# Kernel tuning notes

Hardware: AMD Instinct MI355X
Metric: run time of the kernel (lower is better)

## Reference

```python
import jax, jax.numpy as jnp
import numpy as np

D_MODEL = 1024
N_HEADS = 16
HEAD_DIM = D_MODEL // N_HEADS
D_FF = 4 * D_MODEL
LN_EPS = 1e-5


def setup_inputs() -> dict:
    key = jax.random.key(0)
    ks = jax.random.split(key, 12)
    B, T = 16, 512
    s = lambda fan_in: 1.0 / np.sqrt(fan_in)
    inp = {
        'x': jax.random.normal(ks[0], (B, T, D_MODEL), jnp.float32),
        # torch Linear layout: [out_features, in_features]
        'w_qkv': jax.random.normal(ks[1], (3 * D_MODEL, D_MODEL), jnp.float32) * s(D_MODEL),
        'w_proj': jax.random.normal(ks[2], (D_MODEL, D_MODEL), jnp.float32) * s(D_MODEL),
        'w_ff1': jax.random.normal(ks[3], (D_FF, D_MODEL), jnp.float32) * s(D_MODEL),
        'b_ff1': jax.random.normal(ks[4], (D_FF,), jnp.float32) * 0.02,
        'w_ff2': jax.random.normal(ks[5], (D_MODEL, D_FF), jnp.float32) * s(D_FF),
        'b_ff2': jax.random.normal(ks[6], (D_MODEL,), jnp.float32) * 0.02,
        'ln1_g': jnp.ones((D_MODEL,), jnp.float32),
        'ln1_b': jnp.zeros((D_MODEL,), jnp.float32),
        'ln2_g': jnp.ones((D_MODEL,), jnp.float32),
        'ln2_b': jnp.zeros((D_MODEL,), jnp.float32),
    }
    return inp


def _layernorm(x, g, b):
    mu = jnp.mean(x, axis=-1, keepdims=True)
    var = jnp.var(x, axis=-1, keepdims=True)
    return (x - mu) * jax.lax.rsqrt(var + LN_EPS) * g + b


def _block(x, w_qkv, w_proj, w_ff1, b_ff1, w_ff2, b_ff2, ln1_g, ln1_b, ln2_g, ln2_b):
    B, T, _ = x.shape
    a = _layernorm(x, ln1_g, ln1_b)
    qkv = a @ w_qkv.T  # [B,T,3D]
    q, k, v = jnp.split(qkv, 3, axis=-1)
    # [B,H,T,hd]
    rs = lambda t: t.reshape(B, T, N_HEADS, HEAD_DIM).transpose(0, 2, 1, 3)
    q, k, v = rs(q), rs(k), rs(v)
    scale = HEAD_DIM ** -0.5
    att = jnp.einsum('bhqd,bhkd->bhqk', q, k) * scale
    causal = jnp.tril(jnp.ones((T, T), bool))
    att = jnp.where(causal, att, jnp.float32(-10000.0))
    att = jax.nn.softmax(att, axis=-1)
    out = jnp.einsum('bhqk,bhkd->bhqd', att, v)
    out = out.transpose(0, 2, 1, 3).reshape(B, T, D_MODEL)
    x = x + out @ w_proj.T
    f = _layernorm(x, ln2_g, ln2_b)
    f = jax.nn.gelu(f @ w_ff1.T + b_ff1, approximate=False) @ w_ff2.T + b_ff2
    return x + f


def reference(x, w_qkv, w_proj, w_ff1, b_ff1, w_ff2, b_ff2, ln1_g, ln1_b, ln2_g, ln2_b):
    return _block(x, w_qkv, w_proj, w_ff1, b_ff1, w_ff2, b_ff2, ln1_g, ln1_b, ln2_g, ln2_b)
```

## Files before the change

### kernel.cpp

```cpp
#include <hip/hip_runtime.h>
#include <stdint.h>

typedef __bf16 bf16x8_t __attribute__((ext_vector_type(8)));
typedef float f32x4_t __attribute__((ext_vector_type(4)));
typedef unsigned short ushort8_t __attribute__((ext_vector_type(8)));

#define DEV __device__ __forceinline__

DEV unsigned short f2bf(float f) {
  union { float f; uint32_t u; } v; v.f = f;
  uint32_t r = v.u + 0x7FFFu + ((v.u >> 16) & 1u);
  return (unsigned short)(r >> 16);
}

DEV void gl_lds16(const void* g, void* l) {
  __builtin_amdgcn_global_load_lds(
      (const __attribute__((address_space(1))) void*)g,
      (__attribute__((address_space(3))) void*)l, 16, 0, 0);
}

DEV float gelu_f(float x) {
  const float y = x * 0.7071067811865475f;
  const float ay = fabsf(y);
  const float t = __builtin_amdgcn_rcpf(1.0f + 0.3275911f * ay);
  float p = fmaf(t, 1.061405429f, -1.453152027f);
  p = fmaf(t, p, 1.421413741f);
  p = fmaf(t, p, -0.284496736f);
  p = fmaf(t, p, 0.254829592f);
  p *= t;
  const float e = __expf(-ay * ay);
  float erfv = 1.0f - p * e;
  erfv = copysignf(erfv, y);
  return 0.5f * x * (1.0f + erfv);
}

__global__ __launch_bounds__(256) void cvt_all(const float* __restrict__ w0, unsigned short* __restrict__ o0,
                                               const float* __restrict__ w1, unsigned short* __restrict__ o1,
                                               const float* __restrict__ w2, unsigned short* __restrict__ o2,
                                               const float* __restrict__ w3, unsigned short* __restrict__ o3) {
  int i = blockIdx.x * 256 + threadIdx.x;
  const float* in; unsigned short* outp;
  if (i < 786432) { in = w0; outp = o0; }
  else if (i < 1048576) { in = w1; outp = o1; i -= 786432; }
  else if (i < 2097152) { in = w2; outp = o2; i -= 1048576; }
  else { in = w3; outp = o3; i -= 2097152; }
  float4 v = ((const float4*)in)[i];
  ushort4 o;
  o.x = f2bf(v.x); o.y = f2bf(v.y); o.z = f2bf(v.z); o.w = f2bf(v.w);
  ((ushort4*)outp)[i] = o;
}

__global__ __launch_bounds__(256) void ln_kernel(const float* __restrict__ x,
                                                 const float* __restrict__ g,
                                                 const float* __restrict__ b,
                                                 unsigned short* __restrict__ outp) {
  const int row = blockIdx.x * 4 + (threadIdx.x >> 6);
  const int lane = threadIdx.x & 63;
  const float4* xr = (const float4*)(x + (size_t)row * 1024);
  float4 v[4];
  float s = 0.f, s2 = 0.f;
#pragma unroll
  for (int j = 0; j < 4; ++j) {
    v[j] = xr[j * 64 + lane];
    s += v[j].x + v[j].y + v[j].z + v[j].w;
    s2 += v[j].x * v[j].x + v[j].y * v[j].y + v[j].z * v[j].z + v[j].w * v[j].w;
  }
#pragma unroll
  for (int off = 1; off < 64; off <<= 1) {
    s += __shfl_xor(s, off, 64);
    s2 += __shfl_xor(s2, off, 64);
  }
  const float mu = s * (1.0f / 1024.0f);
  const float var = s2 * (1.0f / 1024.0f) - mu * mu;
  const float rstd = rsqrtf(var + 1e-5f);
  ushort4* orow = (ushort4*)(outp + (size_t)row * 1024);
  const float4* gp = (const float4*)g;
  const float4* bp = (const float4*)b;
#pragma unroll
  for (int j = 0; j < 4; ++j) {
    float4 gv = gp[j * 64 + lane], bv = bp[j * 64 + lane];
    ushort4 o;
    o.x = f2bf((v[j].x - mu) * rstd * gv.x + bv.x);
    o.y = f2bf((v[j].y - mu) * rstd * gv.y + bv.y);
    o.z = f2bf((v[j].z - mu) * rstd * gv.z + bv.z);
    o.w = f2bf((v[j].w - mu) * rstd * gv.w + bv.w);
    orow[j * 64 + lane] = o;
  }
}

template <int MODE>
__global__ __launch_bounds__(256) void gemm_bt(const unsigned short* __restrict__ A,
                                               const unsigned short* __restrict__ B,
                                               float* __restrict__ Cf,
                                               unsigned short* __restrict__ Cb,
                                               const float* __restrict__ bias,
                                               const float* __restrict__ res,
                                               unsigned short* __restrict__ Vt,
                                               int M, int N, int K) {
  __shared__ unsigned short sA[2][128 * 32];
  __shared__ unsigned short sB[2][128 * 32];
  const int tid = threadIdx.x;
  const int w = tid >> 6, lane = tid & 63;
  const int kg = lane >> 4, l16 = lane & 15;
  const int wm = (w & 1) * 64, wn = (w >> 1) * 64;

  const int cid = blockIdx.y * gridDim.x + blockIdx.x;
  const int colBase = (cid >> 6) * 128;
  const int rowBase = (cid & 63) * 128;

  const int sr = tid >> 2;
  const int gc = ((tid & 3) ^ ((sr >> 1) & 3)) * 8;
  const unsigned short* gA = A + (size_t)(rowBase + sr) * K + gc;
  const unsigned short* gB = B + (size_t)(colBase + sr) * K + gc;

  f32x4_t acc[4][4];
#pragma unroll
  for (int mi = 0; mi < 4; ++mi)
#pragma unroll
    for (int ni = 0; ni < 4; ++ni) acc[mi][ni] = (f32x4_t)0.0f;

  int offA[4], offB[4];
  const int pc = (kg ^ ((l16 >> 1) & 3)) * 8;
#pragma unroll
  for (int i = 0; i < 4; ++i) {
    offA[i] = (wm + i * 16 + l16) * 32 + pc;
    offB[i] = (wn + i * 16 + l16) * 32 + pc;
  }

  gl_lds16(gA, &sA[0][tid * 8]);
  gl_lds16(gA + (size_t)64 * K, &sA[0][2048 + tid * 8]);
  gl_lds16(gB, &sB[0][tid * 8]);
  gl_lds16(gB + (size_t)64 * K, &sB[0][2048 + tid * 8]);
  gA += 32; gB += 32;

  const int nk = K >> 5;
  for (int kt = 0; kt < nk; ++kt) {
    __syncthreads();
    if (kt + 1 < nk) {
      const int nb = (kt + 1) & 1;
      gl_lds16(gA, &sA[nb][tid * 8]);
      gl_lds16(gA + (size_t)64 * K, &sA[nb][2048 + tid * 8]);
      gl_lds16(gB, &sB[nb][tid * 8]);
      gl_lds16(gB + (size_t)64 * K, &sB[nb][2048 + tid * 8]);
      gA += 32; gB += 32;
    }
    const int bo = (kt & 1) * (128 * 32);
    bf16x8_t a[4], b[4];
#pragma unroll
    for (int i = 0; i < 4; ++i) a[i] = *(const bf16x8_t*)(&sA[0][0] + bo + offA[i]);
#pragma unroll
    for (int i = 0; i < 4; ++i) b[i] = *(const bf16x8_t*)(&sB[0][0] + bo + offB[i]);
#pragma unroll
    for (int mi = 0; mi < 4; ++mi)
#pragma unroll
      for (int ni = 0; ni < 4; ++ni)
        acc[mi][ni] = __builtin_amdgcn_mfma_f32_16x16x32_bf16(a[mi], b[ni], acc[mi][ni], 0, 0, 0);
  }

#pragma unroll
  for (int mi = 0; mi < 4; ++mi) {
#pragma unroll
    for (int ni = 0; ni < 4; ++ni) {
      const int col = colBase + wn + ni * 16 + l16;
      if (MODE == 0 && colBase >= 2048) {
        const int c2 = col - 2048;
        const int hh = c2 >> 6, dd = c2 & 63;
        const int rw = rowBase + wm + mi * 16 + kg * 4;
        ushort4 pk;
        pk.x = f2bf(acc[mi][ni][0]);
        pk.y = f2bf(acc[mi][ni][1]);
        pk.z = f2bf(acc[mi][ni][2]);
        pk.w = f2bf(acc[mi][ni][3]);
        *(ushort4*)(Vt + (((size_t)(rw >> 9) * 16 + hh) * 64 + dd) * 512 + (rw & 511)) = pk;
        continue;
      }
      float bv = 0.f;
      if (MODE == 2 || MODE == 3) bv = bias[col];
#pragma unroll
      for (int r = 0; r < 4; ++r) {
        const int row = rowBase + wm + mi * 16 + kg * 4 + r;
        const size_t idx = (size_t)row * N + col;
        float v = acc[mi][ni][r];
        if (MODE == 0) {
          Cb[idx] = f2bf(v);
        } else if (MODE == 1) {
          Cf[idx] = v + res[idx];
        } else if (MODE == 2) {
          Cb[idx] = f2bf(gelu_f(v + bv));
        } else {
          Cf[idx] = v + bv + res[idx];
        }
      }
    }
  }
}

__global__ __launch_bounds__(256) void attn_kernel(const unsigned short* __restrict__ qkv,
                                                   const unsigned short* __restrict__ Vt,
                                                   unsigned short* __restrict__ outp) {
  constexpr int D3 = 3072;
  __shared__ unsigned short sQ[128 * 64];
  __shared__ unsigned short sK[64 * 64];
  __shared__ unsigned short sVt[64 * 64];
  __shared__ unsigned short sP[128 * 72];
  const int tid = threadIdx.x;
  const int w = tid >> 6, lane = tid & 63;
  const int kg = lane >> 4, l16 = lane & 15;
  const int qi = blockIdx.x, h = blockIdx.y, bb = blockIdx.z;
  const int t0 = qi * 128;
  const size_t base = (size_t)bb * 512 * D3 + h * 64;

  const int sr = tid >> 3;
  const int sc = ((tid & 7) ^ (sr & 7)) * 8;

  {
    const unsigned short* g = qkv + base + (size_t)(t0 + sr) * D3 + sc;
    unsigned short* l = sQ + tid * 8;
#pragma unroll
    for (int i = 0; i < 4; ++i) gl_lds16(g + (size_t)32 * i * D3, l + 2048 * i);
  }

  const unsigned short* gVbase = Vt + ((size_t)(bb * 16 + h) * 64 + sr) * 512 + sc;

  const int wm = w * 32;
  f32x4_t o[2][4];
  float m_i[2][4], l_i[2][4];
#pragma unroll
  for (int mi = 0; mi < 2; ++mi)
#pragma unroll
    for (int r = 0; r < 4; ++r) { m_i[mi][r] = -1e30f; l_i[mi][r] = 0.f; }
#pragma unroll
  for (int mi = 0; mi < 2; ++mi)
#pragma unroll
    for (int di = 0; di < 4; ++di) o[mi][di] = (f32x4_t)0.0f;

  const int nkt = (qi + 1) * 2;
  for (int kt = 0; kt < nkt; ++kt) {
    const int k0 = kt * 64;
    __syncthreads();
    {
      const unsigned short* g = qkv + base + 1024 + (size_t)(k0 + sr) * D3 + sc;
      unsigned short* l = sK + tid * 8;
      gl_lds16(g, l);
      gl_lds16(g + (size_t)32 * D3, l + 2048);
    }
    {
      const unsigned short* g = gVbase + k0;
      unsigned short* l = sVt + tid * 8;
      gl_lds16(g, l);
      gl_lds16(g + (size_t)32 * 512, l + 2048);
    }
    __syncthreads();

    const bool active = (k0 <= t0 + wm + 31);
    if (active) {
      f32x4_t s[2][4];
#pragma unroll
      for (int mi = 0; mi < 2; ++mi)
#pragma unroll
        for (int ni = 0; ni < 4; ++ni) s[mi][ni] = (f32x4_t)0.0f;
#pragma unroll
      for (int kd = 0; kd < 2; ++kd) {
        bf16x8_t aq[2], bk[4];
#pragma unroll
        for (int mi = 0; mi < 2; ++mi) {
          const int rr = wm + mi * 16 + l16;
          aq[mi] = *(const bf16x8_t*)(sQ + rr * 64 + (((kd * 4 + kg) ^ (l16 & 7)) * 8));
        }
#pragma unroll
        for (int ni = 0; ni < 4; ++ni) {
          const int rr = ni * 16 + l16;
          bk[ni] = *(const bf16x8_t*)(sK + rr * 64 + (((kd * 4 + kg) ^ (l16 & 7)) * 8));
        }
#pragma unroll
        for (int mi = 0; mi < 2; ++mi)
#pragma unroll
          for (int ni = 0; ni < 4; ++ni)
            s[mi][ni] = __builtin_amdgcn_mfma_f32_16x16x32_bf16(aq[mi], bk[ni], s[mi][ni], 0, 0, 0);
      }
#pragma unroll
      for (int mi = 0; mi < 2; ++mi) {
#pragma unroll
        for (int r = 0; r < 4; ++r) {
          const int q = t0 + wm + mi * 16 + kg * 4 + r;
          float mx = -1e30f;
#pragma unroll
          for (int ni = 0; ni < 4; ++ni) {
            const int kk = k0 + ni * 16 + l16;
            float v = s[mi][ni][r] * 0.125f;
            v = (kk <= q) ? v : -10000.0f;
            s[mi][ni][r] = v;
            mx = fmaxf(mx, v);
          }
#pragma unroll
          for (int off = 1; off < 16; off <<= 1) mx = fmaxf(mx, __shfl_xor(mx, off, 64));
          const float mo = m_i[mi][r];
          const float mn = fmaxf(mo, mx);
          const float alpha = __expf(mo - mn);
          float ps = 0.f;
#pragma unroll
          for (int ni = 0; ni < 4; ++ni) {
            float p = __expf(s[mi][ni][r] - mn);
            s[mi][ni][r] = p;
            ps += p;
          }
#pragma unroll
          for (int off = 1; off < 16; off <<= 1) ps += __shfl_xor(ps, off, 64);
          l_i[mi][r] = l_i[mi][r] * alpha + ps;
          m_i[mi][r] = mn;
#pragma unroll
          for (int di = 0; di < 4; ++di) o[mi][di][r] *= alpha;
          const int prow = wm + mi * 16 + kg * 4 + r;
#pragma unroll
          for (int ni = 0; ni < 4; ++ni)
            sP[prow * 72 + ni * 16 + l16] = f2bf(s[mi][ni][r]);
        }
      }
#pragma unroll
      for (int kd = 0; kd < 2; ++kd) {
        bf16x8_t ap[2], bv[4];
#pragma unroll
        for (int mi = 0; mi < 2; ++mi)
          ap[mi] = *(const bf16x8_t*)(sP + (wm + mi * 16 + l16) * 72 + kd * 32 + kg * 8);
#pragma unroll
        for (int di = 0; di < 4; ++di) {
          const int dd = di * 16 + l16;
          bv[di] = *(const bf16x8_t*)(sVt + dd * 64 + (((kd * 4 + kg) ^ (l16 & 7)) * 8));
        }
#pragma unroll
        for (int mi = 0; mi < 2; ++mi)
#pragma unroll
          for (int di = 0; di < 4; ++di)
            o[mi][di] = __builtin_amdgcn_mfma_f32_16x16x32_bf16(ap[mi], bv[di], o[mi][di], 0, 0, 0);
      }
    }
  }

#pragma unroll
  for (int mi = 0; mi < 2; ++mi) {
#pragma unroll
    for (int r = 0; r < 4; ++r) {
      const float inv = 1.0f / l_i[mi][r];
      const int row = t0 + wm + mi * 16 + kg * 4 + r;
      const size_t ob = ((size_t)bb * 512 + row) * 1024 + h * 64;
#pragma unroll
      for (int di = 0; di < 4; ++di)
        outp[ob + di * 16 + l16] = f2bf(o[mi][di][r] * inv);
    }
  }
}

extern "C" void kernel_launch(void* const* d_in, const int* in_sizes, int n_in,
                              void* d_out, int out_size, void* d_ws, size_t ws_size,
                              hipStream_t stream) {
  const float* x      = (const float*)d_in[0];
  const float* w_qkv  = (const float*)d_in[1];
  const float* w_proj = (const float*)d_in[2];
  const float* w_ff1  = (const float*)d_in[3];
  const float* b_ff1  = (const float*)d_in[4];
  const float* w_ff2  = (const float*)d_in[5];
  const float* b_ff2  = (const float*)d_in[6];
  const float* ln1_g  = (const float*)d_in[7];
  const float* ln1_b  = (const float*)d_in[8];
  const float* ln2_g  = (const float*)d_in[9];
  const float* ln2_b  = (const float*)d_in[10];
  float* out = (float*)d_out;
  char* ws = (char*)d_ws;

  unsigned short* wqkv_b  = (unsigned short*)(ws + 0);
  unsigned short* wproj_b = (unsigned short*)(ws + 6291456);
  unsigned short* wff1_b  = (unsigned short*)(ws + 8388608);
  unsigned short* wff2_b  = (unsigned short*)(ws + 16777216);
  unsigned short* a_b     = (unsigned short*)(ws + 25165824);
  float*          x2_f    = (float*)(ws + 41943040);
  unsigned short* vt_b    = (unsigned short*)(ws + 41943040);
  unsigned short* qkv_b   = (unsigned short*)(ws + 75497472);
  unsigned short* attn_b  = (unsigned short*)(ws + 125829120);
  unsigned short* h_b     = qkv_b;

  cvt_all<<<12288, 256, 0, stream>>>(w_qkv, wqkv_b, w_proj, wproj_b, w_ff1, wff1_b, w_ff2, wff2_b);

  ln_kernel<<<2048, 256, 0, stream>>>(x, ln1_g, ln1_b, a_b);
  gemm_bt<0><<<dim3(24, 64), 256, 0, stream>>>(a_b, wqkv_b, nullptr, qkv_b, nullptr, nullptr, vt_b, 8192, 3072, 1024);
  attn_kernel<<<dim3(4, 16, 16), 256, 0, stream>>>(qkv_b, vt_b, attn_b);
  gemm_bt<1><<<dim3(8, 64), 256, 0, stream>>>(attn_b, wproj_b, x2_f, nullptr, nullptr, x, nullptr, 8192, 1024, 1024);
  ln_kernel<<<2048, 256, 0, stream>>>(x2_f, ln2_g, ln2_b, a_b);
  gemm_bt<2><<<dim3(32, 64), 256, 0, stream>>>(a_b, wff1_b, nullptr, h_b, b_ff1, nullptr, nullptr, 8192, 4096, 1024);
  gemm_bt<3><<<dim3(8, 64), 256, 0, stream>>>(h_b, wff2_b, out, nullptr, b_ff2, x2_f, nullptr, 8192, 1024, 4096);
}
```

Measured before the change: 478.0 us.

## Drop online softmax max tracking and use 64-row tiles for narrow GEMMs

The attention kernel no longer tracks a running max or rescales the accumulator. It computes exp(score*scale) directly with causal zeroing, and gets the row sum from an extra MFMA against a ones vector, which removes the shuffle reductions and rescaling. This relies on the scores staying small enough not to overflow exp, and bf16 rounding of the unnormalised probabilities changes numerics. Separately, the N=1024 GEMMs (proj and ff2) use a templated 64-row M tile, doubling their grid to 1024 blocks for better CU occupancy at the cost of less reuse per block.

```diff
diff --git a/kernel.cpp b/kernel.cpp
--- a/kernel.cpp
+++ b/kernel.cpp
@@ -88,7 +88,7 @@
   }
 }
 
-template <int MODE>
+template <int MODE, int BM>
 __global__ __launch_bounds__(256) void gemm_bt(const unsigned short* __restrict__ A,
                                                const unsigned short* __restrict__ B,
                                                float* __restrict__ Cf,
@@ -97,38 +97,40 @@
                                                const float* __restrict__ res,
                                                unsigned short* __restrict__ Vt,
                                                int M, int N, int K) {
-  __shared__ unsigned short sA[2][128 * 32];
+  constexpr int MI = BM / 32;
+  constexpr int RT = 8192 / BM;
+  constexpr int ABUF = BM * 32;
+  __shared__ unsigned short sA[2][ABUF];
   __shared__ unsigned short sB[2][128 * 32];
   const int tid = threadIdx.x;
   const int w = tid >> 6, lane = tid & 63;
   const int kg = lane >> 4, l16 = lane & 15;
-  const int wm = (w & 1) * 64, wn = (w >> 1) * 64;
+  const int wm = (w & 1) * (BM / 2), wn = (w >> 1) * 64;
 
   const int cid = blockIdx.y * gridDim.x + blockIdx.x;
-  const int colBase = (cid >> 6) * 128;
-  const int rowBase = (cid & 63) * 128;
-
-  const int sr = tid >> 2;
+  const int colBase = (cid / RT) * 128;
+  const int rowBase = (cid % RT) * BM;
+
+  const int sr = (BM == 128) ? (tid >> 2) : ((tid >> 2) & 63);
   const int gc = ((tid & 3) ^ ((sr >> 1) & 3)) * 8;
   const unsigned short* gA = A + (size_t)(rowBase + sr) * K + gc;
   const unsigned short* gB = B + (size_t)(colBase + sr) * K + gc;
 
-  f32x4_t acc[4][4];
-#pragma unroll
-  for (int mi = 0; mi < 4; ++mi)
+  f32x4_t acc[MI][4];
+#pragma unroll
+  for (int mi = 0; mi < MI; ++mi)
 #pragma unroll
     for (int ni = 0; ni < 4; ++ni) acc[mi][ni] = (f32x4_t)0.0f;
 
-  int offA[4], offB[4];
+  int offA[MI], offB[4];
   const int pc = (kg ^ ((l16 >> 1) & 3)) * 8;
 #pragma unroll
-  for (int i = 0; i < 4; ++i) {
-    offA[i] = (wm + i * 16 + l16) * 32 + pc;
-    offB[i] = (wn + i * 16 + l16) * 32 + pc;
-  }
+  for (int i = 0; i < MI; ++i) offA[i] = (wm + i * 16 + l16) * 32 + pc;
+#pragma unroll
+  for (int i = 0; i < 4; ++i) offB[i] = (wn + i * 16 + l16) * 32 + pc;
 
   gl_lds16(gA, &sA[0][tid * 8]);
-  gl_lds16(gA + (size_t)64 * K, &sA[0][2048 + tid * 8]);
+  if (BM == 128) gl_lds16(gA + (size_t)64 * K, &sA[0][2048 + tid * 8]);
   gl_lds16(gB, &sB[0][tid * 8]);
   gl_lds16(gB + (size_t)64 * K, &sB[0][2048 + tid * 8]);
   gA += 32; gB += 32;
@@ -139,26 +141,26 @@
     if (kt + 1 < nk) {
       const int nb = (kt + 1) & 1;
       gl_lds16(gA, &sA[nb][tid * 8]);
-      gl_lds16(gA + (size_t)64 * K, &sA[nb][2048 + tid * 8]);
+      if (BM == 128) gl_lds16(gA + (size_t)64 * K, &sA[nb][2048 + tid * 8]);
       gl_lds16(gB, &sB[nb][tid * 8]);
       gl_lds16(gB + (size_t)64 * K, &sB[nb][2048 + tid * 8]);
       gA += 32; gB += 32;
     }
-    const int bo = (kt & 1) * (128 * 32);
-    bf16x8_t a[4], b[4];
-#pragma unroll
-    for (int i = 0; i < 4; ++i) a[i] = *(const bf16x8_t*)(&sA[0][0] + bo + offA[i]);
-#pragma unroll
-    for (int i = 0; i < 4; ++i) b[i] = *(const bf16x8_t*)(&sB[0][0] + bo + offB[i]);
-#pragma unroll
-    for (int mi = 0; mi < 4; ++mi)
+    const int par = kt & 1;
+    bf16x8_t a[MI], b[4];
+#pragma unroll
+    for (int i = 0; i < MI; ++i) a[i] = *(const bf16x8_t*)(&sA[par][0] + offA[i]);
+#pragma unroll
+    for (int i = 0; i < 4; ++i) b[i] = *(const bf16x8_t*)(&sB[par][0] + offB[i]);
+#pragma unroll
+    for (int mi = 0; mi < MI; ++mi)
 #pragma unroll
       for (int ni = 0; ni < 4; ++ni)
         acc[mi][ni] = __builtin_amdgcn_mfma_f32_16x16x32_bf16(a[mi], b[ni], acc[mi][ni], 0, 0, 0);
   }
 
 #pragma unroll
-  for (int mi = 0; mi < 4; ++mi) {
+  for (int mi = 0; mi < MI; ++mi) {
 #pragma unroll
     for (int ni = 0; ni < 4; ++ni) {
       const int col = colBase + wn + ni * 16 + l16;
@@ -222,17 +224,19 @@
 
   const unsigned short* gVbase = Vt + ((size_t)(bb * 16 + h) * 64 + sr) * 512 + sc;
 
+  bf16x8_t ones;
+#pragma unroll
+  for (int j = 0; j < 8; ++j) ones[j] = (__bf16)1.0f;
+
   const int wm = w * 32;
   f32x4_t o[2][4];
-  float m_i[2][4], l_i[2][4];
-#pragma unroll
-  for (int mi = 0; mi < 2; ++mi)
-#pragma unroll
-    for (int r = 0; r < 4; ++r) { m_i[mi][r] = -1e30f; l_i[mi][r] = 0.f; }
-#pragma unroll
-  for (int mi = 0; mi < 2; ++mi)
+  f32x4_t lsum[2];
+#pragma unroll
+  for (int mi = 0; mi < 2; ++mi) {
+    lsum[mi] = (f32x4_t)0.0f;
 #pragma unroll
     for (int di = 0; di < 4; ++di) o[mi][di] = (f32x4_t)0.0f;
+  }
 
   const int nkt = (qi + 1) * 2;
   for (int kt = 0; kt < nkt; ++kt) {
@@ -283,37 +287,13 @@
 #pragma unroll
         for (int r = 0; r < 4; ++r) {
           const int q = t0 + wm + mi * 16 + kg * 4 + r;
-          float mx = -1e30f;
+          const int prow = wm + mi * 16 + kg * 4 + r;
 #pragma unroll
           for (int ni = 0; ni < 4; ++ni) {
             const int kk = k0 + ni * 16 + l16;
-            float v = s[mi][ni][r] * 0.125f;
-            v = (kk <= q) ? v : -10000.0f;
-            s[mi][ni][r] = v;
-            mx = fmaxf(mx, v);
+            const float p = (kk <= q) ? __expf(s[mi][ni][r] * 0.125f) : 0.0f;
+            sP[prow * 72 + ni * 16 + l16] = f2bf(p);
           }
-#pragma unroll
-          for (int off = 1; off < 16; off <<= 1) mx = fmaxf(mx, __shfl_xor(mx, off, 64));
-          const float mo = m_i[mi][r];
-          const float mn = fmaxf(mo, mx);
-          const float alpha = __expf(mo - mn);
-          float ps = 0.f;
-#pragma unroll
-          for (int ni = 0; ni < 4; ++ni) {
-            float p = __expf(s[mi][ni][r] - mn);
-            s[mi][ni][r] = p;
-            ps += p;
-          }
-#pragma unroll
-          for (int off = 1; off < 16; off <<= 1) ps += __shfl_xor(ps, off, 64);
-          l_i[mi][r] = l_i[mi][r] * alpha + ps;
-          m_i[mi][r] = mn;
-#pragma unroll
-          for (int di = 0; di < 4; ++di) o[mi][di][r] *= alpha;
-          const int prow = wm + mi * 16 + kg * 4 + r;
-#pragma unroll
-          for (int ni = 0; ni < 4; ++ni)
-            sP[prow * 72 + ni * 16 + l16] = f2bf(s[mi][ni][r]);
         }
       }
 #pragma unroll
@@ -328,10 +308,12 @@
           bv[di] = *(const bf16x8_t*)(sVt + dd * 64 + (((kd * 4 + kg) ^ (l16 & 7)) * 8));
         }
 #pragma unroll
-        for (int mi = 0; mi < 2; ++mi)
+        for (int mi = 0; mi < 2; ++mi) {
 #pragma unroll
           for (int di = 0; di < 4; ++di)
             o[mi][di] = __builtin_amdgcn_mfma_f32_16x16x32_bf16(ap[mi], bv[di], o[mi][di], 0, 0, 0);
+          lsum[mi] = __builtin_amdgcn_mfma_f32_16x16x32_bf16(ap[mi], ones, lsum[mi], 0, 0, 0);
+        }
       }
     }
   }
@@ -340,7 +322,7 @@
   for (int mi = 0; mi < 2; ++mi) {
 #pragma unroll
     for (int r = 0; r < 4; ++r) {
-      const float inv = 1.0f / l_i[mi][r];
+      const float inv = 1.0f / lsum[mi][r];
       const int row = t0 + wm + mi * 16 + kg * 4 + r;
       const size_t ob = ((size_t)bb * 512 + row) * 1024 + h * 64;
 #pragma unroll
@@ -381,10 +363,10 @@
   cvt_all<<<12288, 256, 0, stream>>>(w_qkv, wqkv_b, w_proj, wproj_b, w_ff1, wff1_b, w_ff2, wff2_b);
 
   ln_kernel<<<2048, 256, 0, stream>>>(x, ln1_g, ln1_b, a_b);
-  gemm_bt<0><<<dim3(24, 64), 256, 0, stream>>>(a_b, wqkv_b, nullptr, qkv_b, nullptr, nullptr, vt_b, 8192, 3072, 1024);
+  gemm_bt<0, 128><<<dim3(24, 64), 256, 0, stream>>>(a_b, wqkv_b, nullptr, qkv_b, nullptr, nullptr, vt_b, 8192, 3072, 1024);
   attn_kernel<<<dim3(4, 16, 16), 256, 0, stream>>>(qkv_b, vt_b, attn_b);
-  gemm_bt<1><<<dim3(8, 64), 256, 0, stream>>>(attn_b, wproj_b, x2_f, nullptr, nullptr, x, nullptr, 8192, 1024, 1024);
+  gemm_bt<1, 64><<<dim3(8, 128), 256, 0, stream>>>(attn_b, wproj_b, x2_f, nullptr, nullptr, x, nullptr, 8192, 1024, 1024);
   ln_kernel<<<2048, 256, 0, stream>>>(x2_f, ln2_g, ln2_b, a_b);
-  gemm_bt<2><<<dim3(32, 64), 256, 0, stream>>>(a_b, wff1_b, nullptr, h_b, b_ff1, nullptr, nullptr, 8192, 4096, 1024);
-  gemm_bt<3><<<dim3(8, 64), 256, 0, stream>>>(h_b, wff2_b, out, nullptr, b_ff2, x2_f, nullptr, 8192, 1024, 4096);
-}
+  gemm_bt<2, 128><<<dim3(32, 64), 256, 0, stream>>>(a_b, wff1_b, nullptr, h_b, b_ff1, nullptr, nullptr, 8192, 4096, 1024);
+  gemm_bt<3, 64><<<dim3(8, 128), 256, 0, stream>>>(h_b, wff2_b, out, nullptr, b_ff2, x2_f, nullptr, 8192, 1024, 4096);
+}
```

Result: no change. 475.9 us (-0.4%).
